# Kernel optimization log

Measured on AMD Instinct MI355X. Metric: run time of the kernel, lower is better.

Reference implementation:

```python
import jax, jax.numpy as jnp
import numpy as np

N = 4096
H_IMG = 512
W_IMG = 512
CHUNK = 128  # gaussians per scan step; N % CHUNK == 0
ALPHA_MAX = 0.999
ALPHA_MIN = 1.0 / 255.0


def setup_inputs() -> dict:
    key = jax.random.key(0)
    k1, k2, k3, k4 = jax.random.split(key, 4)
    _xyz = jax.random.normal(k1, (N, 2), dtype=jnp.float32)          # atanh-space means
    _cholesky = jax.random.uniform(k2, (N, 3), dtype=jnp.float32)    # raw cholesky params
    _features_dc = jax.random.uniform(k3, (N, 3), dtype=jnp.float32)  # RGB colors
    random_colors = jax.random.uniform(k4, (N, 3), dtype=jnp.float32)
    return {"_xyz": _xyz, "_cholesky": _cholesky, "_features_dc": _features_dc,
            "random_colors": random_colors, "H": H_IMG, "W": W_IMG}


def _project(xyz, chol, H, W):
    """project_gaussians_2d: tanh means -> pixel centers, cholesky -> conic."""
    means = jnp.tanh(xyz)                                   # [N,2] in (-1,1)
    L = chol + jnp.asarray([0.5, 0.0, 0.5], chol.dtype)     # cholesky_bound
    l0, l1, l2 = L[:, 0], L[:, 1], L[:, 2]
    # Sigma = L @ L.T with L = [[l0, 0], [l1, l2]]
    s00 = l0 * l0
    s01 = l0 * l1
    s11 = l1 * l1 + l2 * l2
    det = s00 * s11 - s01 * s01
    inv = 1.0 / det
    conics = jnp.stack([s11 * inv, -s01 * inv, s00 * inv], axis=-1)  # [N,3]
    # ndc2pix(v, S) = 0.5 * ((v + 1) * S - 1)
    px = 0.5 * ((means[:, 0] + 1.0) * W - 1.0)
    py = 0.5 * ((means[:, 1] + 1.0) * H - 1.0)
    xys = jnp.stack([px, py], axis=-1)                      # [N,2]
    return xys, conics


def _rasterize_sum(xys, conics, colors, geom_colors, opac, H, W):
    """Accumulated-summation rasterizer: per pixel sum of alpha * color.
    Returns flat [HW,3] rgb, [HW,3] geom rgb, [HW] alpha-sum accumulators."""
    HW = H * W
    p = jnp.arange(HW)
    pxs = (p % W).astype(xys.dtype)   # pixel x coord per flat index
    pys = (p // W).astype(xys.dtype)  # pixel y coord per flat index
    steps = xys.shape[0] // CHUNK

    def rs(a):
        return a.reshape(steps, CHUNK, a.shape[-1])

    chunks = (rs(xys), rs(conics), rs(colors), rs(geom_colors), rs(opac))

    @jax.checkpoint
    def body(carry, ch):
        acc_rgb, acc_geom, acc_a = carry
        cxy, cco, ccol, cgeo, cop = ch
        dx = cxy[:, 0:1] - pxs[None, :]                     # [C, HW]
        dy = cxy[:, 1:2] - pys[None, :]
        sigma = 0.5 * (cco[:, 0:1] * dx * dx + cco[:, 2:3] * dy * dy) + cco[:, 1:2] * dx * dy
        alpha = jnp.minimum(ALPHA_MAX, cop * jnp.exp(-sigma))
        alpha = jnp.where((sigma < 0) | (alpha < ALPHA_MIN), 0.0, alpha)
        acc_rgb = acc_rgb + alpha.T @ ccol                  # [HW,3]
        acc_geom = acc_geom + alpha.T @ cgeo
        acc_a = acc_a + alpha.sum(axis=0)                   # [HW]
        return (acc_rgb, acc_geom, acc_a), None

    z3 = jnp.zeros((HW, 3), xys.dtype)
    za = jnp.zeros((HW,), xys.dtype)
    (acc_rgb, acc_geom, acc_a), _ = jax.lax.scan(body, (z3, z3, za), chunks)
    return acc_rgb, acc_geom, acc_a


def reference(_xyz, _cholesky, _features_dc, random_colors, H, W):
    xys, conics = _project(_xyz, _cholesky, H, W)
    opac = jnp.ones((_xyz.shape[0], 1), _xyz.dtype)         # _opacity buffer, no mask (pruning_mode=None)
    geom_colors = random_colors * 0.5
    acc_rgb, acc_geom, acc_a = _rasterize_sum(xys, conics, _features_dc, geom_colors, opac, H, W)
    render = jnp.clip(acc_rgb, 0.0, 1.0).reshape(1, H, W, 3).transpose(0, 3, 1, 2)
    gauss_render = jnp.clip(acc_geom, 0.0, 1.0).reshape(1, H, W, 3).transpose(0, 3, 1, 2)
    # ones_color rasterization: all 3 channels equal the alpha sum, so mean == acc_a
    alpha_map = acc_a.reshape(1, H, W, 1).transpose(0, 3, 1, 2)
    return render, gauss_render, alpha_map, opac
```

## Files before the change

kernel.cpp:

```cpp
#include <hip/hip_runtime.h>

#define NG 4096
#define W_IMG 512
#define H_IMG 512
#define HW (W_IMG*H_IMG)
#define TILE 16
#define GX (W_IMG/TILE)
#define GY (H_IMG/TILE)

__global__ __launch_bounds__(256) void gs_kernel(
    const float* __restrict__ xyz,
    const float* __restrict__ chol,
    const float* __restrict__ fdc,
    const float* __restrict__ rnd,
    float* __restrict__ out)
{
    __shared__ float sd[256][11];
    __shared__ int scnt;

    const int tid = threadIdx.x;
    const int bx = blockIdx.x % GX;
    const int by = blockIdx.x / GX;
    const int lx = tid & (TILE - 1);
    const int ly = tid >> 4;
    const int gx = bx * TILE + lx;
    const int gy = by * TILE + ly;
    const float fx = (float)gx;
    const float fy = (float)gy;
    const float x0 = (float)(bx * TILE);
    const float x1 = x0 + (float)(TILE - 1);
    const float y0 = (float)(by * TILE);
    const float y1 = y0 + (float)(TILE - 1);

    if (blockIdx.x < NG / 256) out[7 * HW + blockIdx.x * 256 + tid] = 1.0f;

    float ar = 0.f, ag = 0.f, ab = 0.f;
    float br = 0.f, bg = 0.f, bb = 0.f;
    float aa = 0.f;

    if (tid == 0) scnt = 0;
    __syncthreads();

    for (int base = 0; base < NG; base += 256) {
        const int g = base + tid;
        const float2 mxy = *reinterpret_cast<const float2*>(xyz + 2 * g);
        const float px = 0.5f * ((tanhf(mxy.x) + 1.0f) * (float)W_IMG - 1.0f);
        const float py = 0.5f * ((tanhf(mxy.y) + 1.0f) * (float)H_IMG - 1.0f);
        const float l0 = chol[3 * g + 0] + 0.5f;
        const float l1 = chol[3 * g + 1];
        const float l2 = chol[3 * g + 2] + 0.5f;
        const float s00 = l0 * l0;
        const float s01 = l0 * l1;
        const float s11 = l1 * l1 + l2 * l2;
        const float ex = sqrtf(11.0832f * s00) + 0.02f;
        const float ey = sqrtf(11.0832f * s11) + 0.02f;
        if ((px + ex >= x0) && (px - ex <= x1) &&
            (py + ey >= y0) && (py - ey <= y1)) {
            const float det = s00 * s11 - s01 * s01;
            const float inv = 1.0f / det;
            const int pos = atomicAdd(&scnt, 1);
            float* r = sd[pos];
            r[0] = px;  r[1] = py;
            r[2] = s11 * inv;
            r[3] = -s01 * inv;
            r[4] = s00 * inv;
            r[5] = fdc[3 * g + 0]; r[6] = fdc[3 * g + 1]; r[7] = fdc[3 * g + 2];
            r[8] = rnd[3 * g + 0] * 0.5f;
            r[9] = rnd[3 * g + 1] * 0.5f;
            r[10] = rnd[3 * g + 2] * 0.5f;
        }
        __syncthreads();
        const int cnt = scnt;
        for (int k = 0; k < cnt; ++k) {
            const float dx = sd[k][0] - fx;
            const float dy = sd[k][1] - fy;
            const float sig = 0.5f * (sd[k][2] * dx * dx + sd[k][4] * dy * dy)
                              + sd[k][3] * dx * dy;
            float al = fminf(0.999f, __expf(-sig));
            al = ((sig >= 0.0f) && (al >= (1.0f / 255.0f))) ? al : 0.0f;
            ar = fmaf(al, sd[k][5], ar);
            ag = fmaf(al, sd[k][6], ag);
            ab = fmaf(al, sd[k][7], ab);
            br = fmaf(al, sd[k][8], br);
            bg = fmaf(al, sd[k][9], bg);
            bb = fmaf(al, sd[k][10], bb);
            aa += al;
        }
        __syncthreads();
        if (tid == 0) scnt = 0;
        __syncthreads();
    }

    const int p = gy * W_IMG + gx;
    out[0 * HW + p] = fminf(fmaxf(ar, 0.f), 1.f);
    out[1 * HW + p] = fminf(fmaxf(ag, 0.f), 1.f);
    out[2 * HW + p] = fminf(fmaxf(ab, 0.f), 1.f);
    out[3 * HW + p] = fminf(fmaxf(br, 0.f), 1.f);
    out[4 * HW + p] = fminf(fmaxf(bg, 0.f), 1.f);
    out[5 * HW + p] = fminf(fmaxf(bb, 0.f), 1.f);
    out[6 * HW + p] = aa;
}

extern "C" void kernel_launch(void* const* d_in, const int* in_sizes, int n_in,
                              void* d_out, int out_size, void* d_ws, size_t ws_size,
                              hipStream_t stream) {
    const float* xyz  = (const float*)d_in[0];
    const float* chol = (const float*)d_in[1];
    const float* fdc  = (const float*)d_in[2];
    const float* rnd  = (const float*)d_in[3];
    float* out = (float*)d_out;
    gs_kernel<<<GX * GY, 256, 0, stream>>>(xyz, chol, fdc, rnd, out);
}
```

Measured before the change: 87.13 us.

## Split into projection and per-tile binning pass before tile rasterization

Replaces the per-tile culling of all gaussians with one projection kernel. That kernel computes each gaussian's record once and appends its index to per-tile lists with global atomics. The raster kernel then walks only its tile's list and reads packed float4 records from the workspace. This removes the redundant tanh/cholesky math and bounds tests that every tile block did for all 4096 gaussians, and it uses a fast exp-based tanh. In exchange it adds two extra launches, global atomics, unordered lists that change floating-point summation order, and a fixed per-tile capacity that relies on workspace size.

```diff
diff --git a/kernel.cpp b/kernel.cpp
--- a/kernel.cpp
+++ b/kernel.cpp
@@ -7,98 +7,124 @@
 #define TILE 16
 #define GX (W_IMG/TILE)
 #define GY (H_IMG/TILE)
+#define NTILE (GX*GY)
+#define CAP 4096
 
-__global__ __launch_bounds__(256) void gs_kernel(
+
+__device__ __forceinline__ float fast_tanh(float x) {
+    const float ax = fabsf(x);
+    const float e = __expf(-2.0f * ax);
+    const float r = (1.0f - e) / (1.0f + e);
+    return copysignf(r, x);
+}
+
+__global__ __launch_bounds__(256) void zero_kernel(int* __restrict__ cnt) {
+    const int i = blockIdx.x * 256 + threadIdx.x;
+    if (i < NTILE) cnt[i] = 0;
+}
+
+__global__ __launch_bounds__(256) void proj_kernel(
     const float* __restrict__ xyz,
     const float* __restrict__ chol,
     const float* __restrict__ fdc,
     const float* __restrict__ rnd,
+    float4* __restrict__ rec,
+    int* __restrict__ cnt,
+    int* __restrict__ list)
+{
+    const int g = blockIdx.x * 256 + threadIdx.x;
+    const float2 mxy = *reinterpret_cast<const float2*>(xyz + 2 * g);
+    const float px = 0.5f * ((fast_tanh(mxy.x) + 1.0f) * (float)W_IMG - 1.0f);
+    const float py = 0.5f * ((fast_tanh(mxy.y) + 1.0f) * (float)H_IMG - 1.0f);
+    const float l0 = chol[3 * g + 0] + 0.5f;
+    const float l1 = chol[3 * g + 1];
+    const float l2 = chol[3 * g + 2] + 0.5f;
+    const float s00 = l0 * l0;
+    const float s01 = l0 * l1;
+    const float s11 = l1 * l1 + l2 * l2;
+    const float det = s00 * s11 - s01 * s01;
+    const float inv = 1.0f / det;
+
+    rec[g * 3 + 0] = make_float4(px, py, s11 * inv, -s01 * inv);
+    rec[g * 3 + 1] = make_float4(s00 * inv, fdc[3 * g + 0], fdc[3 * g + 1], fdc[3 * g + 2]);
+    rec[g * 3 + 2] = make_float4(rnd[3 * g + 0] * 0.5f, rnd[3 * g + 1] * 0.5f,
+                                 rnd[3 * g + 2] * 0.5f, 0.0f);
+
+    const float ex = sqrtf(11.0832f * s00) + 0.02f;
+    const float ey = sqrtf(11.0832f * s11) + 0.02f;
+    const int tx0 = max(0, (int)floorf((px - ex) * (1.0f / TILE)));
+    const int tx1 = min(GX - 1, (int)floorf((px + ex) * (1.0f / TILE)));
+    const int ty0 = max(0, (int)floorf((py - ey) * (1.0f / TILE)));
+    const int ty1 = min(GY - 1, (int)floorf((py + ey) * (1.0f / TILE)));
+    for (int ty = ty0; ty <= ty1; ++ty)
+        for (int tx = tx0; tx <= tx1; ++tx) {
+            const int t = ty * GX + tx;
+            const int pos = atomicAdd(&cnt[t], 1);
+            list[t * CAP + pos] = g;
+        }
+}
+
+__global__ __launch_bounds__(256) void raster_kernel(
+    const float4* __restrict__ rec,
+    const int* __restrict__ cnt,
+    const int* __restrict__ list,
     float* __restrict__ out)
 {
-    __shared__ float sd[256][11];
-    __shared__ int scnt;
+    __shared__ float4 sd[256][3];
 
+    const int t = blockIdx.x;
     const int tid = threadIdx.x;
-    const int bx = blockIdx.x % GX;
-    const int by = blockIdx.x / GX;
-    const int lx = tid & (TILE - 1);
-    const int ly = tid >> 4;
-    const int gx = bx * TILE + lx;
-    const int gy = by * TILE + ly;
-    const float fx = (float)gx;
-    const float fy = (float)gy;
-    const float x0 = (float)(bx * TILE);
-    const float x1 = x0 + (float)(TILE - 1);
-    const float y0 = (float)(by * TILE);
-    const float y1 = y0 + (float)(TILE - 1);
+    const int bx = t % GX;
+    const int by = t / GX;
+    const float fx = (float)(bx * TILE + (tid & (TILE - 1)));
+    const float fy = (float)(by * TILE + (tid >> 4));
 
-    if (blockIdx.x < NG / 256) out[7 * HW + blockIdx.x * 256 + tid] = 1.0f;
+    if (t < NG / 256) out[7 * HW + t * 256 + tid] = 1.0f;
 
     float ar = 0.f, ag = 0.f, ab = 0.f;
     float br = 0.f, bg = 0.f, bb = 0.f;
     float aa = 0.f;
 
-    if (tid == 0) scnt = 0;
-    __syncthreads();
-
-    for (int base = 0; base < NG; base += 256) {
-        const int g = base + tid;
-        const float2 mxy = *reinterpret_cast<const float2*>(xyz + 2 * g);
-        const float px = 0.5f * ((tanhf(mxy.x) + 1.0f) * (float)W_IMG - 1.0f);
-        const float py = 0.5f * ((tanhf(mxy.y) + 1.0f) * (float)H_IMG - 1.0f);
-        const float l0 = chol[3 * g + 0] + 0.5f;
-        const float l1 = chol[3 * g + 1];
-        const float l2 = chol[3 * g + 2] + 0.5f;
-        const float s00 = l0 * l0;
-        const float s01 = l0 * l1;
-        const float s11 = l1 * l1 + l2 * l2;
-        const float ex = sqrtf(11.0832f * s00) + 0.02f;
-        const float ey = sqrtf(11.0832f * s11) + 0.02f;
-        if ((px + ex >= x0) && (px - ex <= x1) &&
-            (py + ey >= y0) && (py - ey <= y1)) {
-            const float det = s00 * s11 - s01 * s01;
-            const float inv = 1.0f / det;
-            const int pos = atomicAdd(&scnt, 1);
-            float* r = sd[pos];
-            r[0] = px;  r[1] = py;
-            r[2] = s11 * inv;
-            r[3] = -s01 * inv;
-            r[4] = s00 * inv;
-            r[5] = fdc[3 * g + 0]; r[6] = fdc[3 * g + 1]; r[7] = fdc[3 * g + 2];
-            r[8] = rnd[3 * g + 0] * 0.5f;
-            r[9] = rnd[3 * g + 1] * 0.5f;
-            r[10] = rnd[3 * g + 2] * 0.5f;
+    const int n = cnt[t];
+    for (int base = 0; base < n; base += 256) {
+        const int bc = min(n - base, 256);
+        if (tid < bc) {
+            const int g = list[t * CAP + base + tid];
+            sd[tid][0] = rec[g * 3 + 0];
+            sd[tid][1] = rec[g * 3 + 1];
+            sd[tid][2] = rec[g * 3 + 2];
         }
         __syncthreads();
-        const int cnt = scnt;
-        for (int k = 0; k < cnt; ++k) {
-            const float dx = sd[k][0] - fx;
-            const float dy = sd[k][1] - fy;
-            const float sig = 0.5f * (sd[k][2] * dx * dx + sd[k][4] * dy * dy)
-                              + sd[k][3] * dx * dy;
+        for (int k = 0; k < bc; ++k) {
+            const float4 r0 = sd[k][0];
+            const float4 r1 = sd[k][1];
+            const float4 r2 = sd[k][2];
+            const float dx = r0.x - fx;
+            const float dy = r0.y - fy;
+            const float sig = 0.5f * (r0.z * dx * dx + r1.x * dy * dy)
+                              + r0.w * dx * dy;
             float al = fminf(0.999f, __expf(-sig));
             al = ((sig >= 0.0f) && (al >= (1.0f / 255.0f))) ? al : 0.0f;
-            ar = fmaf(al, sd[k][5], ar);
-            ag = fmaf(al, sd[k][6], ag);
-            ab = fmaf(al, sd[k][7], ab);
-            br = fmaf(al, sd[k][8], br);
-            bg = fmaf(al, sd[k][9], bg);
-            bb = fmaf(al, sd[k][10], bb);
+            ar = fmaf(al, r1.y, ar);
+            ag = fmaf(al, r1.z, ag);
+            ab = fmaf(al, r1.w, ab);
+            br = fmaf(al, r2.x, br);
+            bg = fmaf(al, r2.y, bg);
+            bb = fmaf(al, r2.z, bb);
             aa += al;
         }
         __syncthreads();
-        if (tid == 0) scnt = 0;
-        __syncthreads();
     }
 
-    const int p = gy * W_IMG + gx;
+    const int p = (by * TILE + (tid >> 4)) * W_IMG + bx * TILE + (tid & (TILE - 1));
     out[0 * HW + p] = fminf(fmaxf(ar, 0.f), 1.f);
     out[1 * HW + p] = fminf(fmaxf(ag, 0.f), 1.f);
     out[2 * HW + p] = fminf(fmaxf(ab, 0.f), 1.f);
     out[3 * HW + p] = fminf(fmaxf(br, 0.f), 1.f);
-    out[4 * HW + p] = fminf(fmaxf(bg, 0.f), 1.f);
+    out[4 * HW + p] = fminf(fmaxf(bb, 0.f), 1.f);
     out[5 * HW + p] = fminf(fmaxf(bb, 0.f), 1.f);
     out[6 * HW + p] = aa;
+    out[4 * HW + p] = fminf(fmaxf(bg, 0.f), 1.f);
 }
 
 extern "C" void kernel_launch(void* const* d_in, const int* in_sizes, int n_in,
@@ -109,5 +135,13 @@
     const float* fdc  = (const float*)d_in[2];
     const float* rnd  = (const float*)d_in[3];
     float* out = (float*)d_out;
-    gs_kernel<<<GX * GY, 256, 0, stream>>>(xyz, chol, fdc, rnd, out);
+
+    char* ws = (char*)d_ws;
+    float4* rec = (float4*)(ws);
+    int* cnt    = (int*)(ws + 196608);
+    int* list   = (int*)(ws + 200704);
+
+    zero_kernel<<<(NTILE + 255) / 256, 256, 0, stream>>>(cnt);
+    proj_kernel<<<NG / 256, 256, 0, stream>>>(xyz, chol, fdc, rnd, rec, cnt, list);
+    raster_kernel<<<NTILE, 256, 0, stream>>>(rec, cnt, list, out);
 }
```

New measurement: 75.15 us. -13.7%, faster.
